# Performance work log

Measured on AMD Instinct MI355X. Metric: run time of the kernel, lower is better.

## Reference

```python
import jax, jax.numpy as jnp
import numpy as np

B, TE, TD = 16, 400, 64
E, H = 256, 512
H2 = 2 * H  # 1024
V = 32000


def setup_inputs():
    key = jax.random.key(0)
    k = jax.random.split(key, 16)
    s = 0.05
    return {
        "encoder_inputs": jax.random.randint(k[0], (B, TE), 0, V),
        "decoder_inputs": jax.random.randint(k[1], (B, TD), 0, V),
        "ext_oov_sizes": jax.random.randint(k[2], (B,), 0, 10),
        "enc_idxes_on_ext_voc": jax.random.randint(k[3], (B, TE), 0, V),
        "h0": jnp.zeros((2, B, H), jnp.float32),
        "c0": jnp.zeros((2, B, H), jnp.float32),
        "emb": jax.random.normal(k[4], (V, E)) * 0.1,
        "Wih_f": jax.random.normal(k[5], (4 * H, E)) * s,
        "Whh_f": jax.random.normal(k[6], (4 * H, H)) * s,
        "b_f": jnp.zeros((4 * H,), jnp.float32),
        "Wih_b": jax.random.normal(k[7], (4 * H, E)) * s,
        "Whh_b": jax.random.normal(k[8], (4 * H, H)) * s,
        "b_b": jnp.zeros((4 * H,), jnp.float32),
        "Wih_d": jax.random.normal(k[9], (4 * H2, E + 2 * H2)) * s,
        "Whh_d": jax.random.normal(k[10], (4 * H2, H2)) * s,
        "b_d": jnp.zeros((4 * H2,), jnp.float32),
        "W_ea": jax.random.normal(k[11], (H2, H2)) * 0.006,
        "W_da": jax.random.normal(k[12], (H2, H2)) * 0.006,
        "W_v": jax.random.normal(k[13], (V, 3 * H2)) * s,
        "b_v": jnp.zeros((V,), jnp.float32),
    }


def lstm_cell(x, h, c, Wih, Whh, b):
    z = x @ Wih.T + h @ Whh.T + b
    i, f, g, o = jnp.split(z, 4, axis=-1)
    i, f, o = jax.nn.sigmoid(i), jax.nn.sigmoid(f), jax.nn.sigmoid(o)
    c2 = f * c + i * jnp.tanh(g)
    return o * jnp.tanh(c2), c2


def run_lstm(xs, h0, c0, Wih, Whh, b):
    # xs: [T, B, E]
    def step(carry, x):
        h, c = lstm_cell(x, carry[0], carry[1], Wih, Whh, b)
        return (h, c), h
    (h, c), hs = jax.lax.scan(step, (h0, c0), xs)
    return hs, h, c


def _forward(emb, Wih_f, Whh_f, b_f, Wih_b, Whh_b, b_b, Wih_d, Whh_d, b_d,
             W_ea, W_da, W_v, b_v, h0, c0, encoder_inputs, decoder_inputs):
    xs = emb[encoder_inputs].transpose(1, 0, 2)  # [TE, B, E]
    hs_f, hf, cf = run_lstm(xs, h0[0], c0[0], Wih_f, Whh_f, b_f)
    hs_b, hb, cb = run_lstm(xs[::-1], h0[1], c0[1], Wih_b, Whh_b, b_b)
    enc_out = jnp.concatenate([hs_f, hs_b[::-1]], axis=-1).transpose(1, 0, 2)  # [B, TE, 2H]
    h = jnp.concatenate([hf, hb], axis=-1)  # [B, 2H] (torch reshape of bi-dir last hidden)
    c = jnp.concatenate([cf, cb], axis=-1)
    dec_emb = emb[decoder_inputs].transpose(1, 0, 2)  # [TD, B, E]

    def step(carry, xs_t):
        h, c, accum, buf = carry
        i, emb_t = xs_t
        # intra-temporal encoder attention: exp scores normalized by past accumulation
        scores = jnp.einsum('bd,btd->bt', h @ W_ea, enc_out)  # [B, TE]
        exp_s = jnp.exp(scores)
        denom = jnp.where(i == 0, jnp.ones_like(accum), accum)
        ep = exp_s / denom
        attn = ep / jnp.sum(ep, axis=-1, keepdims=True)
        ctx_e = jnp.einsum('bt,btd->bd', attn, enc_out)
        # intra-decoder attention over previously produced hidden states (masked)
        dsc = jnp.einsum('bd,tbd->bt', h @ W_da, buf)  # [B, TD]
        dsc = jnp.where((jnp.arange(TD) < i)[None, :], dsc, -1e30)
        dw = jnp.where(i == 0, 0.0, jax.nn.softmax(dsc, axis=-1))
        ctx_d = jnp.einsum('bt,tbd->bd', dw, buf)
        x = jnp.concatenate([emb_t, ctx_e, ctx_d], axis=-1)  # [B, E+4H]
        h2, c2 = lstm_cell(x, h, c, Wih_d, Whh_d, b_d)
        buf2 = buf.at[i].set(h2)
        feat = jnp.concatenate([h2, ctx_e, ctx_d], axis=-1)  # [B, 6H]
        logd = jax.nn.log_softmax(feat @ W_v.T + b_v, axis=-1)
        return (h2, c2, accum + exp_s, buf2), logd

    carry0 = (h, c, jnp.zeros((B, TE), h.dtype), jnp.zeros((TD, B, H2), h.dtype))
    (h, c, _, _), logds = jax.lax.scan(step, carry0, (jnp.arange(TD), dec_emb))
    return logds.transpose(1, 0, 2), h[None], c[None]


def reference(encoder_inputs, decoder_inputs, ext_oov_sizes, enc_idxes_on_ext_voc,
              h0, c0, emb, Wih_f, Whh_f, b_f, Wih_b, Whh_b, b_b,
              Wih_d, Whh_d, b_d, W_ea, W_da, W_v, b_v):
    # ext_oov_sizes / enc_idxes_on_ext_voc are unused by forward (as in the torch source)
    return _forward(emb, Wih_f, Whh_f, b_f, Wih_b, Whh_b, b_b, Wih_d, Whh_d, b_d,
                    W_ea, W_da, W_v, b_v, h0, c0, encoder_inputs, decoder_inputs)
```

## Files before the change

kernel.cpp:

```cpp
#include <hip/hip_runtime.h>
#include <math.h>

#define B_  16
#define TE_ 400
#define TD_ 64
#define E_  256
#define H_  512
#define H2_ 1024
#define V_  32000

typedef __attribute__((ext_vector_type(4))) float f32x4;
typedef __attribute__((ext_vector_type(8))) short s16x8;
typedef __attribute__((ext_vector_type(8))) unsigned short u16x8;
typedef __attribute__((ext_vector_type(4))) unsigned short u16x4;

__device__ __forceinline__ float bf2f(unsigned short u){
  union { unsigned int i; float f; } v; v.i = ((unsigned int)u) << 16; return v.f;
}
__device__ __forceinline__ unsigned short f2bf(float f){
  union { float f; unsigned int i; } v; v.f = f;
  return (unsigned short)((v.i + 0x7fffu + ((v.i >> 16) & 1u)) >> 16);
}
__device__ __forceinline__ float sigmoidf_(float x){ return 1.f/(1.f + expf(-x)); }

__device__ __forceinline__ void gl_lds16(const void* gsrc, void* ldst){
  __builtin_amdgcn_global_load_lds(
      (const __attribute__((address_space(1))) unsigned int*)gsrc,
      (__attribute__((address_space(3))) unsigned int*)ldst, 16, 0, 0);
}

__device__ __forceinline__ void arrive8(unsigned* inst){
  __threadfence();
  __hip_atomic_fetch_add(inst + (blockIdx.x & 7u)*16, 1u, __ATOMIC_RELAXED, __HIP_MEMORY_SCOPE_AGENT);
}
__device__ __forceinline__ void poll8(unsigned* inst, unsigned target){
  int it = 0;
  for(;;){
    unsigned s = 0;
    #pragma unroll
    for (int k = 0; k < 8; ++k)
      s += __hip_atomic_load(inst + k*16, __ATOMIC_RELAXED, __HIP_MEMORY_SCOPE_AGENT);
    if (s >= target) break;
    if (it < 6) __builtin_amdgcn_s_sleep(1);
    else if (it < 24) __builtin_amdgcn_s_sleep(4);
    else __builtin_amdgcn_s_sleep(16);
    ++it;
  }
}

__global__ void k_init(unsigned* bars, float* ctxn, float* psumT){
  int gid = blockIdx.x*256 + threadIdx.x;
  if (gid < 81920) bars[gid] = 0u;
  if (gid < 32768) ctxn[gid] = 0.f;
  if (gid < 32) psumT[gid] = 0.f;
}

__global__ void k_gather(const float* __restrict__ emb, const int* __restrict__ idx,
                         unsigned short* __restrict__ out, int T){
  int wv = threadIdx.x >> 6, l = threadIdx.x & 63;
  int row = blockIdx.x*4 + wv;
  if (row >= T*B_) return;
  int t = row >> 4, b = row & 15;
  int tok = idx[b*T + t];
  float4 v = *(const float4*)(emb + (size_t)tok*E_ + l*4);
  u16x4 o; o[0]=f2bf(v.x); o[1]=f2bf(v.y); o[2]=f2bf(v.z); o[3]=f2bf(v.w);
  *(u16x4*)(out + (size_t)row*E_ + l*4) = o;
}

__global__ void k_prep_enc(const float* __restrict__ Wih_f, const float* __restrict__ Whh_f,
                           const float* __restrict__ Wih_b, const float* __restrict__ Whh_b,
                           unsigned short* __restrict__ Wenc){
  int it = blockIdx.x*256 + threadIdx.x;
  int dir = it / (2048*96); int rem = it % (2048*96);
  int pr = rem / 96; int kc = rem % 96; int k0 = kc*8;
  int g = pr >> 6, r = pr & 63, gate = r >> 4, ul = r & 15;
  int orig = gate*H_ + g*16 + ul;
  const float* Wih = dir ? Wih_b : Wih_f;
  const float* Whh = dir ? Whh_b : Whh_f;
  u16x8 o;
  #pragma unroll
  for (int e = 0; e < 8; ++e){
    int k = k0 + e;
    float v = (k < E_) ? Wih[(size_t)orig*E_ + k] : Whh[(size_t)orig*H_ + (k - E_)];
    o[e] = f2bf(v);
  }
  *(u16x8*)(Wenc + ((size_t)dir*2048 + pr)*768 + k0) = o;
}

__device__ __forceinline__ void prep_whext_item(int it, const float* __restrict__ Whh_d,
                                                const float* __restrict__ W_da,
                                                char* __restrict__ WhExt){
  if (it < 524288){
    int g = it >> 13; int rem = it & 8191;
    int kblk = rem >> 10; int rem2 = rem & 1023;
    int row = rem2 >> 4; int k8 = rem2 & 15;
    int gate = row >> 4, ul = row & 15;
    int orig = gate*H2_ + g*16 + ul;
    u16x8 o;
    #pragma unroll
    for (int e = 0; e < 8; ++e)
      o[e] = f2bf(Whh_d[(size_t)orig*H2_ + kblk*128 + k8*8 + e]);
    size_t off = (size_t)g*163840 + (size_t)kblk*20480 + (size_t)(row*256 + ((k8*16) ^ ((row&7)<<4)));
    *(u16x8*)(WhExt + off) = o;
  } else if (it < 655360){
    int qi = it - 524288;
    int g = qi >> 11; int rem = qi & 2047;
    int kblk = rem >> 8; int c2 = rem & 255;
    int wvv = c2 >> 6, rr = (c2 >> 2) & 15, c = c2 & 3;
    int row = g*16 + rr;
    u16x8 o;
    #pragma unroll
    for (int e = 0; e < 8; ++e)
      o[e] = f2bf(W_da[(size_t)row*H2_ + kblk*128 + wvv*32 + c*8 + e]);
    size_t off = (size_t)g*163840 + (size_t)kblk*20480 + 16384
               + (size_t)(wvv*1024 + rr*64 + ((c*16) ^ ((rr&3)<<4)));
    *(u16x8*)(WhExt + off) = o;
  }
}

__device__ __forceinline__ void prep_ctx_item(int it, const float* __restrict__ Wih_d,
                                              char* __restrict__ CtxW){
  int g = it >> 14; int rem = it & 16383;
  int kblk = rem >> 10; int rem2 = rem & 1023;
  int row = rem2 >> 4; int k8 = rem2 & 15;
  int gate = row >> 4, ul = row & 15;
  int orig = gate*H2_ + g*16 + ul;
  int k = 256 + kblk*128 + k8*8;
  u16x8 o;
  #pragma unroll
  for (int e = 0; e < 8; ++e)
    o[e] = f2bf(Wih_d[(size_t)orig*2304 + k + e]);
  size_t off = (size_t)g*262144 + (size_t)kblk*16384 + (size_t)(row*256 + ((k8*16) ^ ((row&7)<<4)));
  *(u16x8*)(CtxW + off) = o;
}

__global__ void k_prep_wihemb(const float* __restrict__ Wih_d, unsigned short* __restrict__ Wemb){
  int it = blockIdx.x*256 + threadIdx.x;
  int p = it >> 5; int k0 = (it & 31)*8;
  int g = p >> 6, gate = (p >> 4) & 3, ul = p & 15;
  int orig = gate*H2_ + g*16 + ul;
  u16x8 o;
  #pragma unroll
  for (int e = 0; e < 8; ++e)
    o[e] = f2bf(Wih_d[(size_t)orig*2304 + k0 + e]);
  *(u16x8*)(Wemb + (size_t)p*256 + k0) = o;
}

__global__ void __launch_bounds__(256, 2) k_zinit(
    const unsigned short* __restrict__ A,
    const unsigned short* __restrict__ Bw,
    const float* __restrict__ bd,
    float* __restrict__ Cz)
{
  __shared__ unsigned short Ab[128*72];
  __shared__ unsigned short Bt[128*72];
  int p = blockIdx.x;
  int mt = p >> 5, nt = p & 31;
  int m0 = mt*128, n0 = nt*128;
  int tid = threadIdx.x, wvv = tid>>6, l = tid&63;
  int wr = wvv>>1, wc = wvv&1;
  f32x4 zero4 = {0.f,0.f,0.f,0.f};
  f32x4 acc[4][4];
  #pragma unroll
  for (int a=0;a<4;++a){
    #pragma unroll
    for (int b=0;b<4;++b) acc[a][b] = zero4;
  }
  for (int k0 = 0; k0 < 256; k0 += 64){
    #pragma unroll
    for (int qq = 0; qq < 4; ++qq){
      int idx8 = (tid + qq*256)*8;
      int r = idx8 >> 6, k = idx8 & 63;
      *(u16x8*)(Ab + r*72 + k) = *(const u16x8*)(A + (size_t)(m0+r)*256 + k0 + k);
      *(u16x8*)(Bt + r*72 + k) = *(const u16x8*)(Bw + (size_t)(n0+r)*256 + k0 + k);
    }
    __syncthreads();
    #pragma unroll
    for (int ks = 0; ks < 2; ++ks){
      s16x8 af[4], bf[4];
      #pragma unroll
      for (int fi=0;fi<4;++fi)
        af[fi] = *(const s16x8*)(Ab + (wr*64+fi*16+(l&15))*72 + ks*32 + (l>>4)*8);
      #pragma unroll
      for (int fj=0;fj<4;++fj)
        bf[fj] = *(const s16x8*)(Bt + (wc*64+fj*16+(l&15))*72 + ks*32 + (l>>4)*8);
      #pragma unroll
      for (int fi=0;fi<4;++fi){
        #pragma unroll
        for (int fj=0;fj<4;++fj)
          acc[fi][fj] = __builtin_amdgcn_mfma_f32_16x16x32_bf16(af[fi], bf[fj], acc[fi][fj], 0,0,0);
      }
    }
    __syncthreads();
  }
  #pragma unroll
  for (int fj=0;fj<4;++fj){
    int col = n0 + wc*64 + fj*16 + (l&15);
    int orig = ((col>>4)&3)*H2_ + (col>>6)*16 + (col&15);
    float bias = bd[orig];
    #pragma unroll
    for (int fi=0;fi<4;++fi){
      #pragma unroll
      for (int j=0;j<4;++j){
        int row = m0 + wr*64 + fi*16 + (l>>4)*4 + j;
        Cz[(size_t)row*4096 + col] = acc[fi][fj][j] + bias;
      }
    }
  }
}

__global__ void __launch_bounds__(256, 2) k_zx(
    const unsigned short* __restrict__ xs,
    const unsigned short* __restrict__ Wenc,
    const float* __restrict__ b_f, const float* __restrict__ b_b,
    unsigned short* __restrict__ zx)
{
  __shared__ unsigned short Ab[128*72];
  __shared__ unsigned short Bt[128*72];
  int pblk = blockIdx.x;
  int dir = pblk / 800; int rem = pblk % 800;
  int mt = rem >> 4, nt = rem & 15;
  int m0 = mt*128, n0 = nt*128;
  int tid = threadIdx.x, wvv = tid>>6, l = tid&63;
  int wr = wvv>>1, wc = wvv&1;
  f32x4 zero4 = {0.f,0.f,0.f,0.f};
  f32x4 acc[4][4];
  #pragma unroll
  for (int a=0;a<4;++a){
    #pragma unroll
    for (int b=0;b<4;++b) acc[a][b] = zero4;
  }
  for (int k0 = 0; k0 < 256; k0 += 64){
    #pragma unroll
    for (int qq = 0; qq < 4; ++qq){
      int idx8 = (tid + qq*256)*8;
      int r = idx8 >> 6, k = idx8 & 63;
      *(u16x8*)(Ab + r*72 + k) = *(const u16x8*)(xs + (size_t)(m0+r)*256 + k0 + k);
      *(u16x8*)(Bt + r*72 + k) = *(const u16x8*)(Wenc + ((size_t)dir*2048 + n0+r)*768 + k0 + k);
    }
    __syncthreads();
    #pragma unroll
    for (int ks = 0; ks < 2; ++ks){
      s16x8 af[4], bf[4];
      #pragma unroll
      for (int fi=0;fi<4;++fi)
        af[fi] = *(const s16x8*)(Ab + (wr*64+fi*16+(l&15))*72 + ks*32 + (l>>4)*8);
      #pragma unroll
      for (int fj=0;fj<4;++fj)
        bf[fj] = *(const s16x8*)(Bt + (wc*64+fj*16+(l&15))*72 + ks*32 + (l>>4)*8);
      #pragma unroll
      for (int fi=0;fi<4;++fi){
        #pragma unroll
        for (int fj=0;fj<4;++fj)
          acc[fi][fj] = __builtin_amdgcn_mfma_f32_16x16x32_bf16(af[fi], bf[fj], acc[fi][fj], 0,0,0);
      }
    }
    __syncthreads();
  }
  const float* bsrc = dir ? b_b : b_f;
  #pragma unroll
  for (int fj=0;fj<4;++fj){
    int col = n0 + wc*64 + fj*16 + (l&15);
    float bias = bsrc[((col>>4)&3)*512 + (col>>6)*16 + (col&15)];
    #pragma unroll
    for (int fi=0;fi<4;++fi){
      #pragma unroll
      for (int j=0;j<4;++j){
        int row = m0 + wr*64 + fi*16 + (l>>4)*4 + j;
        zx[((size_t)dir*6400 + row)*2048 + col] = f2bf(acc[fi][fj][j] + bias);
      }
    }
  }
}

__global__ void __launch_bounds__(256, 2) k_penc(
    const unsigned short* __restrict__ enc,
    const float* __restrict__ Wea,
    unsigned short* __restrict__ P)
{
  __shared__ unsigned short Ab[128*72];
  __shared__ unsigned short Bt[128*72];
  int p = blockIdx.x;
  int mt = p >> 3, nt = p & 7;
  int m0 = mt*128, n0 = nt*128;
  int tid = threadIdx.x, wvv = tid>>6, l = tid&63;
  int wr = wvv>>1, wc = wvv&1;
  f32x4 zero4 = {0.f,0.f,0.f,0.f};
  f32x4 acc[4][4];
  #pragma unroll
  for (int a=0;a<4;++a){
    #pragma unroll
    for (int b=0;b<4;++b) acc[a][b] = zero4;
  }
  for (int k0 = 0; k0 < 1024; k0 += 64){
    #pragma unroll
    for (int qq = 0; qq < 4; ++qq){
      int idx8 = (tid + qq*256)*8;
      int r = idx8 >> 6, k = idx8 & 63;
      *(u16x8*)(Ab + r*72 + k) = *(const u16x8*)(enc + (size_t)(m0+r)*1024 + k0 + k);
    }
    #pragma unroll
    for (int qq = 0; qq < 4; ++qq){
      int idx8 = (tid + qq*256)*8;
      int r = idx8 >> 6, k = idx8 & 63;
      const float* src = Wea + (size_t)(n0+r)*1024 + k0 + k;
      float4 v0 = *(const float4*)src;
      float4 v1 = *(const float4*)(src+4);
      u16x8 o;
      o[0]=f2bf(v0.x); o[1]=f2bf(v0.y); o[2]=f2bf(v0.z); o[3]=f2bf(v0.w);
      o[4]=f2bf(v1.x); o[5]=f2bf(v1.y); o[6]=f2bf(v1.z); o[7]=f2bf(v1.w);
      *(u16x8*)(Bt + r*72 + k) = o;
    }
    __syncthreads();
    #pragma unroll
    for (int ks = 0; ks < 2; ++ks){
      s16x8 af[4], bf[4];
      #pragma unroll
      for (int fi=0;fi<4;++fi)
        af[fi] = *(const s16x8*)(Ab + (wr*64+fi*16+(l&15))*72 + ks*32 + (l>>4)*8);
      #pragma unroll
      for (int fj=0;fj<4;++fj)
        bf[fj] = *(const s16x8*)(Bt + (wc*64+fj*16+(l&15))*72 + ks*32 + (l>>4)*8);
      #pragma unroll
      for (int fi=0;fi<4;++fi){
        #pragma unroll
        for (int fj=0;fj<4;++fj)
          acc[fi][fj] = __builtin_amdgcn_mfma_f32_16x16x32_bf16(af[fi], bf[fj], acc[fi][fj], 0,0,0);
      }
    }
    __syncthreads();
  }
  #pragma unroll
  for (int fj=0;fj<4;++fj){
    int col = n0 + wc*64 + fj*16 + (l&15);
    #pragma unroll
    for (int fi=0;fi<4;++fi){
      #pragma unroll
      for (int j=0;j<4;++j){
        int row = m0 + wr*64 + fi*16 + (l>>4)*4 + j;
        P[(size_t)row*1024 + col] = f2bf(acc[fi][fj][j]);
      }
    }
  }
}

__global__ void __launch_bounds__(256, 1) k_encoder(
    const unsigned short* __restrict__ zx,
    const unsigned short* __restrict__ Wenc,
    const float* __restrict__ h0, const float* __restrict__ c0,
    unsigned short* __restrict__ enc_out,
    unsigned short* __restrict__ hbuf,
    float* __restrict__ h0dec, float* __restrict__ c0dec,
    unsigned* __restrict__ bars,
    const float* __restrict__ Whh_d, const float* __restrict__ W_da,
    const float* __restrict__ Wih_d,
    char* __restrict__ WhExt, char* __restrict__ CtxW)
{
  extern __shared__ char smem[];
  int tid = threadIdx.x;
  int w = blockIdx.x;
  if (w >= 64){
    int base = (w - 64)*256 + tid;
    for (int it = base; it < 655360; it += 36864) prep_whext_item(it, Whh_d, W_da, WhExt);
    for (int it = base; it < 1048576; it += 36864) prep_ctx_item(it, Wih_d, CtxW);
    return;
  }
  unsigned short* Wt = (unsigned short*)smem;
  unsigned short* At = Wt + 64*520;
  float* zl = (float*)(At + 16*520);
  int dir = w >> 5, g = w & 31;
  int wv = tid >> 6, l = tid & 63;
  {
    const unsigned short* Wsrc = Wenc + ((size_t)dir*2048 + g*64)*768 + 256;
    int r = tid >> 2, s = tid & 3;
    for (int c = 0; c < 16; ++c)
      *(u16x8*)(Wt + r*520 + s*128 + c*8) = *(const u16x8*)(Wsrc + (size_t)r*768 + s*128 + c*8);
  }
  int bb = tid >> 4, ul = tid & 15;
  float creg = c0[((size_t)dir*16 + bb)*H_ + g*16 + ul];
  int kchunk = (l >> 4) * 8;
  f32x4 zero4 = { 0.f, 0.f, 0.f, 0.f };
  {
    int r = tid >> 4, s = tid & 15;
    for (int e = 0; e < 32; ++e)
      At[r*520 + s*32 + e] = f2bf(h0[((size_t)dir*16 + r)*H_ + s*32 + e]);
  }
  int tg0 = dir ? (TE_-1) : 0;
  const unsigned short* zrow = zx + ((size_t)dir*6400 + (size_t)tg0*16 + (l>>4)*4)*2048 + g*64 + wv*16 + (l&15);
  f32x4 a0cur;
  a0cur[0]=bf2f(zrow[0]); a0cur[1]=bf2f(zrow[2048]); a0cur[2]=bf2f(zrow[4096]); a0cur[3]=bf2f(zrow[6144]);
  __syncthreads();
  for (int t = 0; t < TE_; ++t){
    int tg = dir ? (TE_-1 - t) : t;
    f32x4 acc0 = a0cur, acc1 = zero4;
    const unsigned short* brow = Wt + (wv*16 + (l&15))*520 + kchunk;
    const unsigned short* ap   = At + (l&15)*520 + kchunk;
    #pragma unroll
    for (int ks = 0; ks < 16; ++ks){
      s16x8 afr = *(const s16x8*)(ap + ks*32);
      s16x8 bfr = *(const s16x8*)(brow + ks*32);
      if (ks & 1) acc1 = __builtin_amdgcn_mfma_f32_16x16x32_bf16(afr, bfr, acc1, 0, 0, 0);
      else        acc0 = __builtin_amdgcn_mfma_f32_16x16x32_bf16(afr, bfr, acc0, 0, 0, 0);
    }
    f32x4 acc = acc0 + acc1;
    #pragma unroll
    for (int j = 0; j < 4; ++j)
      zl[wv*256 + ((l>>4)*4 + j)*16 + (l&15)] = acc[j];
    __syncthreads();
    float zi = zl[0*256 + bb*16 + ul];
    float zf = zl[1*256 + bb*16 + ul];
    float zg = zl[2*256 + bb*16 + ul];
    float zo = zl[3*256 + bb*16 + ul];
    float iv = sigmoidf_(zi), fv = sigmoidf_(zf), gv = tanhf(zg), ov = sigmoidf_(zo);
    float cc = fv*creg + iv*gv;
    float hh = ov * tanhf(cc);
    creg = cc;
    int u = g*16 + ul;
    unsigned short hb = f2bf(hh);
    hbuf[((size_t)dir*2 + ((t+1)&1))*(16*H_) + bb*H_ + u] = hb;
    enc_out[((size_t)bb*TE_ + tg)*H2_ + dir*H_ + u] = hb;
    if (t == TE_-1){
      h0dec[(size_t)bb*H2_ + dir*H_ + u] = hh;
      c0dec[(size_t)bb*H2_ + dir*H_ + u] = cc;
    }
    unsigned* cnt = bars + (size_t)(dir*400 + t)*64;
    __syncthreads();
    if (tid == 0){
      __threadfence();
      __hip_atomic_fetch_add(cnt + (g&3)*16, 1u, __ATOMIC_RELAXED, __HIP_MEMORY_SCOPE_AGENT);
    }
    if (t+1 < TE_){
      int tg2 = dir ? (TE_-2 - t) : (t+1);
      const unsigned short* zr2 = zx + ((size_t)dir*6400 + (size_t)tg2*16 + (l>>4)*4)*2048 + g*64 + wv*16 + (l&15);
      a0cur[0]=bf2f(zr2[0]); a0cur[1]=bf2f(zr2[2048]); a0cur[2]=bf2f(zr2[4096]); a0cur[3]=bf2f(zr2[6144]);
    }
    if (tid == 0){
      int it = 0;
      for(;;){
        unsigned s_ = 0;
        #pragma unroll
        for (int k2 = 0; k2 < 4; ++k2)
          s_ += __hip_atomic_load(cnt + k2*16, __ATOMIC_RELAXED, __HIP_MEMORY_SCOPE_AGENT);
        if (s_ >= 32) break;
        if (it < 6) __builtin_amdgcn_s_sleep(1);
        else __builtin_amdgcn_s_sleep(4);
        ++it;
      }
      __threadfence();
    }
    __syncthreads();
    if (t+1 < TE_){
      int r = tid >> 4, s = tid & 15;
      const unsigned short* hsrc = hbuf + ((size_t)dir*2 + ((t+1)&1))*(16*H_) + r*H_ + s*32;
      for (int c = 0; c < 4; ++c)
        *(u16x8*)(At + r*520 + s*32 + c*8) = *(const u16x8*)(hsrc + c*8);
    }
    __syncthreads();
  }
}

__global__ void k_dec_init(const float* __restrict__ h0dec, unsigned short* __restrict__ hreg){
  int gid = blockIdx.x*256 + threadIdx.x;
  if (gid < 16384) hreg[gid] = f2bf(h0dec[gid]);
}

__device__ __forceinline__ void issueA(const char* gA, char* BbA, int wv, int l, int kblk, int buf){
  const char* gsrc = gA + (size_t)kblk*20480;
  char* lb = BbA + buf*20480;
  #pragma unroll
  for (int q = 0; q < 4; ++q)
    gl_lds16(gsrc + wv*4096 + q*1024 + (size_t)l*16, lb + wv*4096 + q*1024);
  gl_lds16(gsrc + 16384 + wv*1024 + (size_t)l*16, lb + 16384 + wv*1024);
}
__device__ __forceinline__ void issueC(const char* gC, char* BbC, int wv, int l, int kblk, int buf){
  const char* gsrc = gC + (size_t)kblk*16384;
  char* lb = BbC + buf*16384;
  #pragma unroll
  for (int q = 0; q < 4; ++q)
    gl_lds16(gsrc + wv*4096 + q*1024 + (size_t)l*16, lb + wv*4096 + q*1024);
}

__global__ void __launch_bounds__(256, 1) k_decoder(
  const char* __restrict__ WhExt,
  const char* __restrict__ CtxW,
  const float* __restrict__ zinit,
  const unsigned short* __restrict__ Penc,
  const unsigned short* __restrict__ enc_out,
  const float* __restrict__ c0dec,
  unsigned short* __restrict__ hreg,
  unsigned short* __restrict__ xbuf,
  float* __restrict__ ctxn,
  float* __restrict__ psumT,
  unsigned short* __restrict__ vbuf,
  unsigned short* __restrict__ bufh,
  unsigned short* __restrict__ Av,
  float* __restrict__ outHC,
  unsigned* __restrict__ bars)
{
  extern __shared__ char smem[];
  int tid = threadIdx.x, w = blockIdx.x;
  int wv = tid >> 6, l = tid & 63;
  unsigned* dbase = bars + 51200;

  unsigned short* Atc = (unsigned short*)smem;
  unsigned short* Ah  = (unsigned short*)smem;
  char* BbA = smem + 66560;
  char* BbC = smem + 128000;
  float* zq = (float*)(smem + 66560);
  float* zl = (float*)(smem + 128000);
  unsigned short* encL = (unsigned short*)smem;
  float* epL  = (float*)(smem + 103424);
  float* accL = (float*)(smem + 103680);
  float* dscL = (float*)smem;

  bool isZ = (w < 64);
  bool isE = (w >= 64 && w < 192);
  int eb = 0, ec = 0;
  if (isE){ eb = (w-64) >> 3; ec = (w-64) & 7; }
  int db = w - 192;

  if (isE){
    for (int rr = 0; rr < 50; ++rr){
      const unsigned short* src = enc_out + ((size_t)eb*TE_ + ec*50 + rr)*H2_;
      *(u16x4*)(encL + rr*1032 + tid*4) = *(const u16x4*)(src + tid*4);
    }
    if (tid < 50) accL[tid] = 0.f;
    __syncthreads();
  }
  float creg = 0.f;
  int bb = tid >> 4, ul = tid & 15;
  const char* gA = WhExt + (size_t)w*163840;
  const char* gC = CtxW + (size_t)w*262144;
  f32x4 acc0, acc1;

  for (int i = 0; i < TD_; ++i){
    int p = i & 1;
    unsigned* barM = dbase + (size_t)(i*3+0)*128;
    unsigned* barA = dbase + (size_t)(i*3+1)*128;
    unsigned* barB = dbase + (size_t)(i*3+2)*128;

    if (isZ){
      ctxn[(p^1)*16384 + w*256 + tid] = 0.f;
      if (w == 0 && tid < 16) psumT[(p^1)*16 + tid] = 0.f;
      const float* zsrc = zinit + ((size_t)i*16 + (l>>4)*4)*4096 + w*64 + wv*16 + (l&15);
      f32x4 a0i; a0i[0]=zsrc[0]; a0i[1]=zsrc[4096]; a0i[2]=zsrc[8192]; a0i[3]=zsrc[12288];
      issueA(gA, BbA, wv, l, 0, 0);
      issueA(gA, BbA, wv, l, 1, 1);
      {
        int r = tid >> 4, s = tid & 15;
        const unsigned short* hsrc = hreg + p*16384 + r*H2_ + s*64;
        for (int c = 0; c < 8; ++c)
          *(u16x8*)(Ah + r*1032 + s*64 + c*8) = *(const u16x8*)(hsrc + c*8);
      }
      __syncthreads();
      acc0 = a0i;
      f32x4 z4 = {0.f,0.f,0.f,0.f};
      acc1 = z4;
      f32x4 accv = z4;
      int swz = ((l&7)<<4);
      for (int kblk = 0; kblk < 8; ++kblk){
        int buf = kblk % 3;
        if (kblk + 2 < 8) issueA(gA, BbA, wv, l, kblk+2, (kblk+2)%3);
        if (kblk < 6)       asm volatile("s_waitcnt vmcnt(10)" ::: "memory");
        else if (kblk == 6) asm volatile("s_waitcnt vmcnt(5)" ::: "memory");
        else                asm volatile("s_waitcnt vmcnt(0)" ::: "memory");
        const unsigned short* ap = Ah + (l&15)*1032 + kblk*128 + (l>>4)*8;
        const char* Bz = BbA + buf*20480 + wv*4096;
        #pragma unroll
        for (int ks = 0; ks < 4; ++ks){
          int k8 = ks*4 + (l>>4);
          s16x8 afr = *(const s16x8*)(ap + ks*32);
          s16x8 bfr = *(const s16x8*)(Bz + (l&15)*256 + ((k8*16) ^ swz));
          if (ks & 1) acc1 = __builtin_amdgcn_mfma_f32_16x16x32_bf16(afr, bfr, acc1, 0,0,0);
          else        acc0 = __builtin_amdgcn_mfma_f32_16x16x32_bf16(afr, bfr, acc0, 0,0,0);
        }
        s16x8 afq = *(const s16x8*)(Ah + (l&15)*1032 + kblk*128 + wv*32 + (l>>4)*8);
        s16x8 bfv = *(const s16x8*)(BbA + buf*20480 + 16384 + wv*1024 + (l&15)*64 + ((((l>>4)*16)) ^ ((l&3)<<4)));
        accv = __builtin_amdgcn_mfma_f32_16x16x32_bf16(afq, bfv, accv, 0,0,0);
      }
      __syncthreads();
      #pragma unroll
      for (int j = 0; j < 4; ++j)
        zq[wv*256 + ((l>>4)*4+j)*16 + (l&15)] = accv[j];
      __syncthreads();
      if (i > 0){
        float vv = zq[0*256+bb*16+ul] + zq[1*256+bb*16+ul] + zq[2*256+bb*16+ul] + zq[3*256+bb*16+ul];
        vbuf[((size_t)(i-1)*16 + bb)*H2_ + w*16 + ul] = f2bf(vv);
      }
      __syncthreads();
      if (tid == 0) arrive8(barM);
      issueC(gC, BbC, wv, l, 0, 0);
      issueC(gC, BbC, wv, l, 1, 1);
      if (tid == 0){ poll8(barA, 144); __threadfence(); }
      __syncthreads();
      {
        int r = tid >> 4, s = tid & 15;
        float inv = 1.f / psumT[p*16 + r];
        const float* cn = ctxn + p*16384 + (size_t)r*1024 + s*64;
        for (int c8 = 0; c8 < 8; ++c8){
          float4 v0 = *(const float4*)(cn + c8*8);
          float4 v1 = *(const float4*)(cn + c8*8 + 4);
          u16x8 o;
          o[0]=f2bf(v0.x*inv); o[1]=f2bf(v0.y*inv); o[2]=f2bf(v0.z*inv); o[3]=f2bf(v0.w*inv);
          o[4]=f2bf(v1.x*inv); o[5]=f2bf(v1.y*inv); o[6]=f2bf(v1.z*inv); o[7]=f2bf(v1.w*inv);
          *(u16x8*)(Atc + r*2056 + s*64 + c8*8) = o;
        }
        const unsigned short* xd = xbuf + (size_t)r*1024 + s*64;
        for (int c8 = 0; c8 < 8; ++c8)
          *(u16x8*)(Atc + r*2056 + 1024 + s*64 + c8*8) = *(const u16x8*)(xd + c8*8);
      }
      {
        float val = ctxn[p*16384 + (size_t)bb*1024 + w*16 + ul] / psumT[p*16 + bb];
        Av[((size_t)bb*TD_ + i)*3072 + 1024 + w*16 + ul] = f2bf(val);
      }
      __syncthreads();
      for (int k = 0; k < 16; ++k){
        if (k < 15) asm volatile("s_waitcnt vmcnt(4)" ::: "memory");
        else        asm volatile("s_waitcnt vmcnt(0)" ::: "memory");
        const unsigned short* ap = Atc + (l&15)*2056 + k*128 + (l>>4)*8;
        const char* Bz = BbC + (k&1)*16384 + wv*4096;
        #pragma unroll
        for (int ks = 0; ks < 4; ++ks){
          int k8 = ks*4 + (l>>4);
          s16x8 afr = *(const s16x8*)(ap + ks*32);
          s16x8 bfr = *(const s16x8*)(Bz + (l&15)*256 + ((k8*16) ^ swz));
          if (ks & 1) acc1 = __builtin_amdgcn_mfma_f32_16x16x32_bf16(afr, bfr, acc1, 0,0,0);
          else        acc0 = __builtin_amdgcn_mfma_f32_16x16x32_bf16(afr, bfr, acc0, 0,0,0);
        }
        if (k + 2 < 16) issueC(gC, BbC, wv, l, k+2, k&1);
      }
      __syncthreads();
      f32x4 acc = acc0 + acc1;
      #pragma unroll
      for (int j = 0; j < 4; ++j)
        zl[wv*256 + ((l>>4)*4+j)*16 + (l&15)] = acc[j];
      __syncthreads();
      float zi = zl[0*256 + bb*16 + ul];
      float zf = zl[1*256 + bb*16 + ul];
      float zg = zl[2*256 + bb*16 + ul];
      float zo = zl[3*256 + bb*16 + ul];
      if (i == 0) creg = c0dec[(size_t)bb*H2_ + w*16 + ul];
      float iv = sigmoidf_(zi), fv = sigmoidf_(zf), gv = tanhf(zg), ov = sigmoidf_(zo);
      float cc = fv*creg + iv*gv;
      float hh = ov*tanhf(cc);
      creg = cc;
      int u = w*16 + ul;
      unsigned short hb2 = f2bf(hh);
      hreg[((i+1)&1)*16384 + (size_t)bb*H2_ + u] = hb2;
      Av[((size_t)bb*TD_ + i)*3072 + u] = hb2;
      bufh[((size_t)i*16 + bb)*H2_ + u] = hb2;
      if (i == TD_-1){
        outHC[(size_t)bb*H2_ + u] = hh;
        outHC[16384 + (size_t)bb*H2_ + u] = cc;
      }
      __syncthreads();
      if (tid == 0){ arrive8(barB); poll8(barB, 64); __threadfence(); }
      __syncthreads();
    } else if (isE){
      const unsigned short* hb_ = hreg + p*16384 + eb*H2_ + l*16;
      u16x8 hv0 = *(const u16x8*)hb_;
      u16x8 hv1 = *(const u16x8*)(hb_ + 8);
      float hf[16];
      #pragma unroll
      for (int c = 0; c < 8; ++c){ hf[c] = bf2f(hv0[c]); hf[8+c] = bf2f(hv1[c]); }
      for (int rr = wv; rr < 50; rr += 4){
        const unsigned short* pr = Penc + ((size_t)(eb*TE_ + ec*50 + rr))*H2_ + l*16;
        u16x8 p0 = *(const u16x8*)pr;
        u16x8 p1 = *(const u16x8*)(pr + 8);
        float sc = 0.f;
        #pragma unroll
        for (int c = 0; c < 8; ++c) sc += hf[c]*bf2f(p0[c]);
        #pragma unroll
        for (int c = 0; c < 8; ++c) sc += hf[8+c]*bf2f(p1[c]);
        #pragma unroll
        for (int o = 1; o < 64; o <<= 1) sc += __shfl_xor(sc, o);
        if (l == 0){
          float es = expf(sc);
          float aold = accL[rr];
          float denom = (i == 0) ? 1.f : aold;
          accL[rr] = aold + es;
          epL[rr] = es / denom;
        }
      }
      __syncthreads();
      float tot = 0.f;
      for (int rr = 0; rr < 50; ++rr) tot += epL[rr];
      float a0=0.f,a1=0.f,a2=0.f,a3=0.f;
      for (int rr = 0; rr < 50; ++rr){
        float wgt = epL[rr];
        u16x4 ev = *(const u16x4*)(encL + rr*1032 + tid*4);
        a0 += wgt*bf2f(ev[0]); a1 += wgt*bf2f(ev[1]); a2 += wgt*bf2f(ev[2]); a3 += wgt*bf2f(ev[3]);
      }
      float* dst = ctxn + p*16384 + (size_t)eb*1024 + tid*4;
      atomicAdd(dst+0, a0); atomicAdd(dst+1, a1); atomicAdd(dst+2, a2); atomicAdd(dst+3, a3);
      if (tid == 0) atomicAdd(psumT + p*16 + eb, tot);
      __syncthreads();
      if (tid == 0){ arrive8(barA); poll8(barB, 64); __threadfence(); }
      __syncthreads();
    } else {
      int col = tid*4;
      if (i == 0){
        u16x4 z4v = {0,0,0,0};
        *(u16x4*)(xbuf + (size_t)db*1024 + col) = z4v;
        *(u16x4*)(Av + ((size_t)db*TD_ + i)*3072 + 2048 + col) = z4v;
      } else {
        if (tid == 0){ poll8(barM, 64); __threadfence(); }
        __syncthreads();
        const unsigned short* hq = hreg + p*16384 + db*H2_ + l*16;
        u16x8 h0v = *(const u16x8*)hq;
        u16x8 h1v = *(const u16x8*)(hq + 8);
        float qf[16];
        #pragma unroll
        for (int c = 0; c < 8; ++c){ qf[c] = bf2f(h0v[c]); qf[8+c] = bf2f(h1v[c]); }
        for (int tp = wv; tp < i; tp += 4){
          const unsigned short* vr = vbuf + ((size_t)tp*16 + db)*H2_ + l*16;
          u16x8 e0 = *(const u16x8*)vr;
          u16x8 e1 = *(const u16x8*)(vr + 8);
          float sc = 0.f;
          #pragma unroll
          for (int c = 0; c < 8; ++c) sc += qf[c]*bf2f(e0[c]);
          #pragma unroll
          for (int c = 0; c < 8; ++c) sc += qf[8+c]*bf2f(e1[c]);
          #pragma unroll
          for (int o = 1; o < 64; o <<= 1) sc += __shfl_xor(sc, o);
          if (l == 0) dscL[tp] = sc;
        }
        __syncthreads();
        float scv = (l < i) ? dscL[l] : -1e30f;
        float m = scv;
        #pragma unroll
        for (int o = 1; o < 64; o <<= 1) m = fmaxf(m, __shfl_xor(m, o));
        float e = (l < i) ? expf(scv - m) : 0.f;
        float ssum = e;
        #pragma unroll
        for (int o = 1; o < 64; o <<= 1) ssum += __shfl_xor(ssum, o);
        float wgt = e / ssum;
        float c0_=0.f,c1_=0.f,c2_=0.f,c3_=0.f;
        for (int tp = 0; tp < i; ++tp){
          float wt = __shfl(wgt, tp);
          u16x4 hv = *(const u16x4*)(bufh + ((size_t)tp*16 + db)*H2_ + col);
          c0_ += wt*bf2f(hv[0]); c1_ += wt*bf2f(hv[1]); c2_ += wt*bf2f(hv[2]); c3_ += wt*bf2f(hv[3]);
        }
        u16x4 o4; o4[0]=f2bf(c0_); o4[1]=f2bf(c1_); o4[2]=f2bf(c2_); o4[3]=f2bf(c3_);
        *(u16x4*)(xbuf + (size_t)db*1024 + col) = o4;
        *(u16x4*)(Av + ((size_t)db*TD_ + i)*3072 + 2048 + col) = o4;
      }
      __syncthreads();
      if (tid == 0){ arrive8(barA); poll8(barB, 64); __threadfence(); }
      __syncthreads();
    }
  }
}

__global__ void __launch_bounds__(256, 2) k_vocab_gemm(
    const unsigned short* __restrict__ Av,
    const float* __restrict__ Wv,
    const float* __restrict__ bv,
    float* __restrict__ out)
{
  __shared__ unsigned short Ab[128*72];
  __shared__ unsigned short Bt[128*72];
  int p = blockIdx.x;
  int mt = (p>>3)&7, nt = (p&7) + 8*(p>>6);
  if (nt >= 250) return;
  int m0 = mt*128, n0 = nt*128;
  int tid = threadIdx.x, wvv = tid>>6, l = tid&63;
  int wr = wvv>>1, wc = wvv&1;
  f32x4 zero4 = {0.f,0.f,0.f,0.f};
  f32x4 acc[4][4];
  #pragma unroll
  for (int a=0;a<4;++a){
    #pragma unroll
    for (int b=0;b<4;++b) acc[a][b] = zero4;
  }
  for (int k0 = 0; k0 < 3072; k0 += 64){
    #pragma unroll
    for (int qq = 0; qq < 4; ++qq){
      int idx8 = (tid + qq*256)*8;
      int r = idx8 >> 6, k = idx8 & 63;
      *(u16x8*)(Ab + r*72 + k) = *(const u16x8*)(Av + (size_t)(m0+r)*3072 + k0 + k);
    }
    #pragma unroll
    for (int qq = 0; qq < 4; ++qq){
      int idx8 = (tid + qq*256)*8;
      int r = idx8 >> 6, k = idx8 & 63;
      const float* src = Wv + (size_t)(n0+r)*3072 + k0 + k;
      float4 v0 = *(const float4*)src;
      float4 v1 = *(const float4*)(src+4);
      u16x8 o;
      o[0]=f2bf(v0.x); o[1]=f2bf(v0.y); o[2]=f2bf(v0.z); o[3]=f2bf(v0.w);
      o[4]=f2bf(v1.x); o[5]=f2bf(v1.y); o[6]=f2bf(v1.z); o[7]=f2bf(v1.w);
      *(u16x8*)(Bt + r*72 + k) = o;
    }
    __syncthreads();
    #pragma unroll
    for (int ks = 0; ks < 2; ++ks){
      s16x8 af[4], bf[4];
      #pragma unroll
      for (int fi=0;fi<4;++fi)
        af[fi] = *(const s16x8*)(Ab + (wr*64+fi*16+(l&15))*72 + ks*32 + (l>>4)*8);
      #pragma unroll
      for (int fj=0;fj<4;++fj)
        bf[fj] = *(const s16x8*)(Bt + (wc*64+fj*16+(l&15))*72 + ks*32 + (l>>4)*8);
      #pragma unroll
      for (int fi=0;fi<4;++fi){
        #pragma unroll
        for (int fj=0;fj<4;++fj)
          acc[fi][fj] = __builtin_amdgcn_mfma_f32_16x16x32_bf16(af[fi], bf[fj], acc[fi][fj], 0,0,0);
      }
    }
    __syncthreads();
  }
  #pragma unroll
  for (int fj=0;fj<4;++fj){
    int col = n0 + wc*64 + fj*16 + (l&15);
    float bias = bv[col];
    #pragma unroll
    for (int fi=0;fi<4;++fi){
      #pragma unroll
      for (int j=0;j<4;++j){
        int row = m0 + wr*64 + fi*16 + (l>>4)*4 + j;
        out[(size_t)row*V_ + col] = acc[fi][fj][j] + bias;
      }
    }
  }
}

__global__ void k_logsoftmax(float* __restrict__ out){
  int row = blockIdx.x;
  float* x = out + (size_t)row*V_;
  int tid = threadIdx.x;
  __shared__ float red[64];
  float m = -1e30f;
  for (int c = tid; c < V_; c += 256) m = fmaxf(m, x[c]);
  #pragma unroll
  for (int o=1;o<64;o<<=1) m = fmaxf(m, __shfl_xor(m,o));
  if ((tid&63)==0) red[tid>>6] = m;
  __syncthreads();
  m = fmaxf(fmaxf(red[0],red[1]), fmaxf(red[2],red[3]));
  float s = 0.f;
  for (int c = tid; c < V_; c += 256) s += expf(x[c]-m);
  #pragma unroll
  for (int o=1;o<64;o<<=1) s += __shfl_xor(s,o);
  if ((tid&63)==0) red[8 + (tid>>6)] = s;
  __syncthreads();
  s = red[8]+red[9]+red[10]+red[11];
  float lse = m + logf(s);
  for (int c = tid; c < V_; c += 256) x[c] = x[c] - lse;
}

extern "C" void kernel_launch(void* const* d_in, const int* in_sizes, int n_in,
                              void* d_out, int out_size, void* d_ws, size_t ws_size,
                              hipStream_t stream){
  (void)in_sizes; (void)n_in; (void)out_size; (void)ws_size;
  const int*   enc_in = (const int*)d_in[0];
  const int*   dec_in = (const int*)d_in[1];
  const float* h0   = (const float*)d_in[4];
  const float* c0   = (const float*)d_in[5];
  const float* emb  = (const float*)d_in[6];
  const float* Wih_f= (const float*)d_in[7];
  const float* Whh_f= (const float*)d_in[8];
  const float* b_f  = (const float*)d_in[9];
  const float* Wih_b= (const float*)d_in[10];
  const float* Whh_b= (const float*)d_in[11];
  const float* b_b  = (const float*)d_in[12];
  const float* Wih_d= (const float*)d_in[13];
  const float* Whh_d= (const float*)d_in[14];
  const float* b_d  = (const float*)d_in[15];
  const float* W_ea = (const float*)d_in[16];
  const float* W_da = (const float*)d_in[17];
  const float* W_v  = (const float*)d_in[18];
  const float* b_v  = (const float*)d_in[19];
  float* out = (float*)d_out;
  char* ws = (char*)d_ws;

  size_t o_bars   = 0;
  size_t o_ctxn   = 327680;
  size_t o_psumT  = o_ctxn + 131072;
  size_t o_xs     = o_psumT + 256;
  size_t o_decemb = o_xs + (size_t)6400*256*2;
  size_t o_Wenc   = o_decemb + (size_t)1024*256*2;
  size_t o_WhExt  = o_Wenc + (size_t)2*2048*768*2;
  size_t o_CtxW   = o_WhExt + (size_t)64*163840;
  size_t o_Wemb   = o_CtxW + (size_t)64*262144;
  size_t o_zinit  = o_Wemb + (size_t)4096*256*2;
  size_t o_zx     = o_zinit + (size_t)1024*4096*4;
  size_t o_enc    = o_zx + (size_t)2*6400*2048*2;
  size_t o_Penc   = o_enc + (size_t)16*400*1024*2;
  size_t o_hbuf   = o_Penc + (size_t)16*400*1024*2;
  size_t o_h0dec  = o_hbuf + (size_t)2*2*16*512*2;
  size_t o_c0dec  = o_h0dec + (size_t)16*1024*4;
  size_t o_hreg   = o_c0dec + (size_t)16*1024*4;
  size_t o_xbuf   = o_hreg + (size_t)2*16*1024*2;
  size_t o_vbuf   = o_xbuf + (size_t)16*1024*2;
  size_t o_bufh   = o_vbuf + (size_t)64*16*1024*2;
  size_t o_Av     = o_bufh + (size_t)64*16*1024*2;

  unsigned* bars        = (unsigned*)(ws + o_bars);
  float* ctxn           = (float*)(ws + o_ctxn);
  float* psumT          = (float*)(ws + o_psumT);
  unsigned short* xs    = (unsigned short*)(ws + o_xs);
  unsigned short* decemb= (unsigned short*)(ws + o_decemb);
  unsigned short* Wenc  = (unsigned short*)(ws + o_Wenc);
  char* WhExt           = ws + o_WhExt;
  char* CtxW            = ws + o_CtxW;
  unsigned short* Wemb  = (unsigned short*)(ws + o_Wemb);
  float* zinit          = (float*)(ws + o_zinit);
  unsigned short* zx    = (unsigned short*)(ws + o_zx);
  unsigned short* encO  = (unsigned short*)(ws + o_enc);
  unsigned short* Penc  = (unsigned short*)(ws + o_Penc);
  unsigned short* hbuf  = (unsigned short*)(ws + o_hbuf);
  float* h0dec          = (float*)(ws + o_h0dec);
  float* c0dec          = (float*)(ws + o_c0dec);
  unsigned short* hreg  = (unsigned short*)(ws + o_hreg);
  unsigned short* xbuf  = (unsigned short*)(ws + o_xbuf);
  unsigned short* vbuf  = (unsigned short*)(ws + o_vbuf);
  unsigned short* bufh  = (unsigned short*)(ws + o_bufh);
  unsigned short* Av    = (unsigned short*)(ws + o_Av);

  hipFuncSetAttribute((const void*)k_encoder, hipFuncAttributeMaxDynamicSharedMemorySize, 90000);
  hipFuncSetAttribute((const void*)k_decoder, hipFuncAttributeMaxDynamicSharedMemorySize, 160768);

  k_init<<<320, 256, 0, stream>>>(bars, ctxn, psumT);
  k_gather<<<1600, 256, 0, stream>>>(emb, enc_in, xs, TE_);
  k_gather<<<256, 256, 0, stream>>>(emb, dec_in, decemb, TD_);
  k_prep_enc<<<1536, 256, 0, stream>>>(Wih_f, Whh_f, Wih_b, Whh_b, Wenc);
  k_prep_wihemb<<<512, 256, 0, stream>>>(Wih_d, Wemb);
  k_zinit<<<256, 256, 0, stream>>>(decemb, Wemb, b_d, zinit);
  k_zx<<<1600, 256, 0, stream>>>(xs, Wenc, b_f, b_b, zx);
  k_encoder<<<208, 256, 87296, stream>>>(zx, Wenc, h0, c0, encO, hbuf, h0dec, c0dec, bars,
                                         Whh_d, W_da, Wih_d, WhExt, CtxW);
  k_penc<<<400, 256, 0, stream>>>(encO, W_ea, Penc);
  k_dec_init<<<64, 256, 0, stream>>>(h0dec, hreg);
  k_decoder<<<208, 256, 160768, stream>>>(WhExt, CtxW, zinit, Penc, encO, c0dec,
                                          hreg, xbuf, ctxn, psumT, vbuf, bufh, Av,
                                          out + (size_t)32768000, bars);
  k_vocab_gemm<<<2048, 256, 0, stream>>>(Av, W_v, b_v, out);
  k_logsoftmax<<<1024, 256, 0, stream>>>(out);
}
```

Measured before the change: 5.538 ms.

## Restructure decoder into 256 uniform blocks with resident Whh slices

The decoder moves from a 208-block heterogeneous split (gate-GEMM, attention and decoder-attention roles) to 256 uniform blocks. Each block owns 4 hidden units, keeps its Whh_d slice and its slice of the projected encoder output in LDS, and streams its context weights each step. The W_da projection becomes an fp32 dot product with cross-lane reductions instead of an MFMA tile. Barrier counters are re-laid out per instance and spread over 8 slots, and weight prep and permutations are rewritten to match. This targets per-step latency and load imbalance in the serial decoder loop, at the cost of more blocks joining each grid barrier and scalar fp32 work in place of MFMA.

```diff
diff --git a/kernel.cpp b/kernel.cpp
--- a/kernel.cpp
+++ b/kernel.cpp
@@ -28,29 +28,35 @@
       (const __attribute__((address_space(1))) unsigned int*)gsrc,
       (__attribute__((address_space(3))) unsigned int*)ldst, 16, 0, 0);
 }
-
-__device__ __forceinline__ void arrive8(unsigned* inst){
+__device__ __forceinline__ void issue4(const char* gsrc, char* ldst, int l){
+  #pragma unroll
+  for (int q = 0; q < 4; ++q)
+    gl_lds16(gsrc + q*1024 + (size_t)l*16, ldst + q*1024);
+}
+
+__device__ __forceinline__ void d_arrive(unsigned* bars, int inst){
   __threadfence();
-  __hip_atomic_fetch_add(inst + (blockIdx.x & 7u)*16, 1u, __ATOMIC_RELAXED, __HIP_MEMORY_SCOPE_AGENT);
-}
-__device__ __forceinline__ void poll8(unsigned* inst, unsigned target){
+  __hip_atomic_fetch_add(bars + (blockIdx.x & 7u)*4096 + inst*16, 1u, __ATOMIC_RELAXED, __HIP_MEMORY_SCOPE_AGENT);
+}
+__device__ __forceinline__ void d_poll(unsigned* bars, int inst, unsigned tgt){
   int it = 0;
   for(;;){
     unsigned s = 0;
     #pragma unroll
     for (int k = 0; k < 8; ++k)
-      s += __hip_atomic_load(inst + k*16, __ATOMIC_RELAXED, __HIP_MEMORY_SCOPE_AGENT);
-    if (s >= target) break;
+      s += __hip_atomic_load(bars + k*4096 + inst*16, __ATOMIC_RELAXED, __HIP_MEMORY_SCOPE_AGENT);
+    if (s >= tgt) break;
     if (it < 6) __builtin_amdgcn_s_sleep(1);
     else if (it < 24) __builtin_amdgcn_s_sleep(4);
     else __builtin_amdgcn_s_sleep(16);
     ++it;
   }
+  __threadfence();
 }
 
 __global__ void k_init(unsigned* bars, float* ctxn, float* psumT){
   int gid = blockIdx.x*256 + threadIdx.x;
-  if (gid < 81920) bars[gid] = 0u;
+  if (gid < 99328) bars[gid] = 0u;
   if (gid < 32768) ctxn[gid] = 0.f;
   if (gid < 32) psumT[gid] = 0.f;
 }
@@ -87,58 +93,38 @@
   *(u16x8*)(Wenc + ((size_t)dir*2048 + pr)*768 + k0) = o;
 }
 
-__device__ __forceinline__ void prep_whext_item(int it, const float* __restrict__ Whh_d,
-                                                const float* __restrict__ W_da,
-                                                char* __restrict__ WhExt){
-  if (it < 524288){
-    int g = it >> 13; int rem = it & 8191;
-    int kblk = rem >> 10; int rem2 = rem & 1023;
-    int row = rem2 >> 4; int k8 = rem2 & 15;
-    int gate = row >> 4, ul = row & 15;
-    int orig = gate*H2_ + g*16 + ul;
-    u16x8 o;
-    #pragma unroll
-    for (int e = 0; e < 8; ++e)
-      o[e] = f2bf(Whh_d[(size_t)orig*H2_ + kblk*128 + k8*8 + e]);
-    size_t off = (size_t)g*163840 + (size_t)kblk*20480 + (size_t)(row*256 + ((k8*16) ^ ((row&7)<<4)));
-    *(u16x8*)(WhExt + off) = o;
-  } else if (it < 655360){
-    int qi = it - 524288;
-    int g = qi >> 11; int rem = qi & 2047;
-    int kblk = rem >> 8; int c2 = rem & 255;
-    int wvv = c2 >> 6, rr = (c2 >> 2) & 15, c = c2 & 3;
-    int row = g*16 + rr;
-    u16x8 o;
-    #pragma unroll
-    for (int e = 0; e < 8; ++e)
-      o[e] = f2bf(W_da[(size_t)row*H2_ + kblk*128 + wvv*32 + c*8 + e]);
-    size_t off = (size_t)g*163840 + (size_t)kblk*20480 + 16384
-               + (size_t)(wvv*1024 + rr*64 + ((c*16) ^ ((rr&3)<<4)));
-    *(u16x8*)(WhExt + off) = o;
-  }
-}
-
-__device__ __forceinline__ void prep_ctx_item(int it, const float* __restrict__ Wih_d,
-                                              char* __restrict__ CtxW){
-  int g = it >> 14; int rem = it & 16383;
-  int kblk = rem >> 10; int rem2 = rem & 1023;
-  int row = rem2 >> 4; int k8 = rem2 & 15;
-  int gate = row >> 4, ul = row & 15;
-  int orig = gate*H2_ + g*16 + ul;
-  int k = 256 + kblk*128 + k8*8;
+__device__ __forceinline__ void prep_rwhh_item(int it, const float* __restrict__ Whh_d,
+                                               char* __restrict__ RW){
+  int w = it >> 11; int rem = it & 2047;
+  int sb = rem >> 8; int e = rem & 255;
+  int row = e >> 4, k8 = e & 15;
+  int orig = (row >> 2)*H2_ + w*4 + (row & 3);
   u16x8 o;
   #pragma unroll
-  for (int e = 0; e < 8; ++e)
-    o[e] = f2bf(Wih_d[(size_t)orig*2304 + k + e]);
-  size_t off = (size_t)g*262144 + (size_t)kblk*16384 + (size_t)(row*256 + ((k8*16) ^ ((row&7)<<4)));
-  *(u16x8*)(CtxW + off) = o;
+  for (int e2 = 0; e2 < 8; ++e2)
+    o[e2] = f2bf(Whh_d[(size_t)orig*H2_ + sb*128 + k8*8 + e2]);
+  size_t off = (size_t)w*32768 + (size_t)sb*4096 + (size_t)(row*256 + ((k8*16) ^ ((row&7)<<4)));
+  *(u16x8*)(RW + off) = o;
+}
+__device__ __forceinline__ void prep_rwctx_item(int it, const float* __restrict__ Wih_d,
+                                                char* __restrict__ RC){
+  int w = it >> 12; int rem = it & 4095;
+  int sb = rem >> 8; int e = rem & 255;
+  int row = e >> 4, k8 = e & 15;
+  int orig = (row >> 2)*H2_ + w*4 + (row & 3);
+  int col = 256 + sb*128 + k8*8;
+  u16x8 o;
+  #pragma unroll
+  for (int e2 = 0; e2 < 8; ++e2)
+    o[e2] = f2bf(Wih_d[(size_t)orig*2304 + col + e2]);
+  size_t off = (size_t)w*65536 + (size_t)sb*4096 + (size_t)(row*256 + ((k8*16) ^ ((row&7)<<4)));
+  *(u16x8*)(RC + off) = o;
 }
 
 __global__ void k_prep_wihemb(const float* __restrict__ Wih_d, unsigned short* __restrict__ Wemb){
   int it = blockIdx.x*256 + threadIdx.x;
   int p = it >> 5; int k0 = (it & 31)*8;
-  int g = p >> 6, gate = (p >> 4) & 3, ul = p & 15;
-  int orig = gate*H2_ + g*16 + ul;
+  int orig = ((p>>2)&3)*H2_ + (p>>4)*4 + (p&3);
   u16x8 o;
   #pragma unroll
   for (int e = 0; e < 8; ++e)
@@ -196,7 +182,7 @@
   #pragma unroll
   for (int fj=0;fj<4;++fj){
     int col = n0 + wc*64 + fj*16 + (l&15);
-    int orig = ((col>>4)&3)*H2_ + (col>>6)*16 + (col&15);
+    int orig = ((col>>2)&3)*H2_ + (col>>4)*4 + (col&3);
     float bias = bd[orig];
     #pragma unroll
     for (int fi=0;fi<4;++fi){
@@ -352,17 +338,16 @@
     unsigned short* __restrict__ hbuf,
     float* __restrict__ h0dec, float* __restrict__ c0dec,
     unsigned* __restrict__ bars,
-    const float* __restrict__ Whh_d, const float* __restrict__ W_da,
-    const float* __restrict__ Wih_d,
-    char* __restrict__ WhExt, char* __restrict__ CtxW)
+    const float* __restrict__ Whh_d, const float* __restrict__ Wih_d,
+    char* __restrict__ RWhhG, char* __restrict__ RWctxG)
 {
   extern __shared__ char smem[];
   int tid = threadIdx.x;
   int w = blockIdx.x;
   if (w >= 64){
     int base = (w - 64)*256 + tid;
-    for (int it = base; it < 655360; it += 36864) prep_whext_item(it, Whh_d, W_da, WhExt);
-    for (int it = base; it < 1048576; it += 36864) prep_ctx_item(it, Wih_d, CtxW);
+    for (int it = base; it < 524288; it += 36864) prep_rwhh_item(it, Whh_d, RWhhG);
+    for (int it = base; it < 1048576; it += 36864) prep_rwctx_item(it, Wih_d, RWctxG);
     return;
   }
   unsigned short* Wt = (unsigned short*)smem;
@@ -370,6 +355,7 @@
   float* zl = (float*)(At + 16*520);
   int dir = w >> 5, g = w & 31;
   int wv = tid >> 6, l = tid & 63;
+  unsigned* ebars = bars + 32768;
   {
     const unsigned short* Wsrc = Wenc + ((size_t)dir*2048 + g*64)*768 + 256;
     int r = tid >> 2, s = tid & 3;
@@ -423,11 +409,11 @@
       h0dec[(size_t)bb*H2_ + dir*H_ + u] = hh;
       c0dec[(size_t)bb*H2_ + dir*H_ + u] = cc;
     }
-    unsigned* cnt = bars + (size_t)(dir*400 + t)*64;
+    int inst = dir*400 + t;
     __syncthreads();
     if (tid == 0){
       __threadfence();
-      __hip_atomic_fetch_add(cnt + (g&3)*16, 1u, __ATOMIC_RELAXED, __HIP_MEMORY_SCOPE_AGENT);
+      __hip_atomic_fetch_add(ebars + (g&3)*16384 + inst*16, 1u, __ATOMIC_RELAXED, __HIP_MEMORY_SCOPE_AGENT);
     }
     if (t+1 < TE_){
       int tg2 = dir ? (TE_-2 - t) : (t+1);
@@ -440,7 +426,7 @@
         unsigned s_ = 0;
         #pragma unroll
         for (int k2 = 0; k2 < 4; ++k2)
-          s_ += __hip_atomic_load(cnt + k2*16, __ATOMIC_RELAXED, __HIP_MEMORY_SCOPE_AGENT);
+          s_ += __hip_atomic_load(ebars + k2*16384 + inst*16, __ATOMIC_RELAXED, __HIP_MEMORY_SCOPE_AGENT);
         if (s_ >= 32) break;
         if (it < 6) __builtin_amdgcn_s_sleep(1);
         else __builtin_amdgcn_s_sleep(4);
@@ -464,28 +450,21 @@
   if (gid < 16384) hreg[gid] = f2bf(h0dec[gid]);
 }
 
-__device__ __forceinline__ void issueA(const char* gA, char* BbA, int wv, int l, int kblk, int buf){
-  const char* gsrc = gA + (size_t)kblk*20480;
-  char* lb = BbA + buf*20480;
-  #pragma unroll
-  for (int q = 0; q < 4; ++q)
-    gl_lds16(gsrc + wv*4096 + q*1024 + (size_t)l*16, lb + wv*4096 + q*1024);
-  gl_lds16(gsrc + 16384 + wv*1024 + (size_t)l*16, lb + 16384 + wv*1024);
-}
-__device__ __forceinline__ void issueC(const char* gC, char* BbC, int wv, int l, int kblk, int buf){
-  const char* gsrc = gC + (size_t)kblk*16384;
-  char* lb = BbC + buf*16384;
-  #pragma unroll
-  for (int q = 0; q < 4; ++q)
-    gl_lds16(gsrc + wv*4096 + q*1024 + (size_t)l*16, lb + wv*4096 + q*1024);
-}
+#define OFF_PENC  32768
+#define OFF_WB    83968
+#define OFF_ZL    149504
+#define OFF_EPL   157696
+#define OFF_ACCL  157824
+#define OFF_DSCL  157952
+#define DEC_SMEM  158208
 
 __global__ void __launch_bounds__(256, 1) k_decoder(
-  const char* __restrict__ WhExt,
-  const char* __restrict__ CtxW,
+  const char* __restrict__ RWhhG,
+  const char* __restrict__ RWctxG,
   const float* __restrict__ zinit,
   const unsigned short* __restrict__ Penc,
   const unsigned short* __restrict__ enc_out,
+  const float* __restrict__ W_da,
   const float* __restrict__ c0dec,
   unsigned short* __restrict__ hreg,
   unsigned short* __restrict__ xbuf,
@@ -498,180 +477,120 @@
   unsigned* __restrict__ bars)
 {
   extern __shared__ char smem[];
+  char* RW = smem;
+  unsigned short* PencL = (unsigned short*)(smem + OFF_PENC);
+  char* WB = smem + OFF_WB;
+  float* zl   = (float*)(smem + OFF_ZL);
+  float* epL  = (float*)(smem + OFF_EPL);
+  float* accL = (float*)(smem + OFF_ACCL);
+  float* dscL = (float*)(smem + OFF_DSCL);
+
   int tid = threadIdx.x, w = blockIdx.x;
   int wv = tid >> 6, l = tid & 63;
-  unsigned* dbase = bars + 51200;
-
-  unsigned short* Atc = (unsigned short*)smem;
-  unsigned short* Ah  = (unsigned short*)smem;
-  char* BbA = smem + 66560;
-  char* BbC = smem + 128000;
-  float* zq = (float*)(smem + 66560);
-  float* zl = (float*)(smem + 128000);
-  unsigned short* encL = (unsigned short*)smem;
-  float* epL  = (float*)(smem + 103424);
-  float* accL = (float*)(smem + 103680);
-  float* dscL = (float*)smem;
-
-  bool isZ = (w < 64);
-  bool isE = (w >= 64 && w < 192);
-  int eb = 0, ec = 0;
-  if (isE){ eb = (w-64) >> 3; ec = (w-64) & 7; }
-  int db = w - 192;
-
-  if (isE){
-    for (int rr = 0; rr < 50; ++rr){
-      const unsigned short* src = enc_out + ((size_t)eb*TE_ + ec*50 + rr)*H2_;
-      *(u16x4*)(encL + rr*1032 + tid*4) = *(const u16x4*)(src + tid*4);
-    }
-    if (tid < 50) accL[tid] = 0.f;
-    __syncthreads();
-  }
+  int b_att = w >> 4, tr = w & 15;
+  bool isDec = ((w & 3) == 0);
+  int qd = (w >> 2) & 3, b_dec = w >> 4;
+  int swz = ((l&7)<<4);
+
+  {
+    const float4* src = (const float4*)(RWhhG + (size_t)w*32768);
+    float4* dst = (float4*)RW;
+    for (int o = tid; o < 2048; o += 256) dst[o] = src[o];
+    const float4* ps = (const float4*)(Penc + ((size_t)b_att*400 + tr*25)*1024);
+    float4* pd = (float4*)PencL;
+    for (int o = tid; o < 3200; o += 256) pd[o] = ps[o];
+  }
+  if (tid < 25) accL[tid] = 0.f;
   float creg = 0.f;
-  int bb = tid >> 4, ul = tid & 15;
-  const char* gA = WhExt + (size_t)w*163840;
-  const char* gC = CtxW + (size_t)w*262144;
-  f32x4 acc0, acc1;
+  if (tid < 64) creg = c0dec[(size_t)(tid>>2)*H2_ + w*4 + (tid&3)];
+  __syncthreads();
+
+  const char* gWB = RWctxG + (size_t)w*65536;
+  char* myWB = WB + wv*16384;
 
   for (int i = 0; i < TD_; ++i){
     int p = i & 1;
-    unsigned* barM = dbase + (size_t)(i*3+0)*128;
-    unsigned* barA = dbase + (size_t)(i*3+1)*128;
-    unsigned* barB = dbase + (size_t)(i*3+2)*128;
-
-    if (isZ){
+    int instV = i*3, instX = i*3+1, instY = i*3+2;
+    if (w < 64){
       ctxn[(p^1)*16384 + w*256 + tid] = 0.f;
       if (w == 0 && tid < 16) psumT[(p^1)*16 + tid] = 0.f;
-      const float* zsrc = zinit + ((size_t)i*16 + (l>>4)*4)*4096 + w*64 + wv*16 + (l&15);
-      f32x4 a0i; a0i[0]=zsrc[0]; a0i[1]=zsrc[4096]; a0i[2]=zsrc[8192]; a0i[3]=zsrc[12288];
-      issueA(gA, BbA, wv, l, 0, 0);
-      issueA(gA, BbA, wv, l, 1, 1);
-      {
-        int r = tid >> 4, s = tid & 15;
-        const unsigned short* hsrc = hreg + p*16384 + r*H2_ + s*64;
-        for (int c = 0; c < 8; ++c)
-          *(u16x8*)(Ah + r*1032 + s*64 + c*8) = *(const u16x8*)(hsrc + c*8);
-      }
-      __syncthreads();
-      acc0 = a0i;
+    }
+    issue4(gWB + (size_t)(2*wv+0)*4096, myWB + 0*4096, l);
+    issue4(gWB + (size_t)(2*wv+1)*4096, myWB + 1*4096, l);
+    issue4(gWB + (size_t)(8+2*wv)*4096, myWB + 2*4096, l);
+    issue4(gWB + (size_t)(9+2*wv)*4096, myWB + 3*4096, l);
+    if (i > 0){
+      for (int bi = 0; bi < 4; ++bi){
+        int b2 = wv*4 + bi;
+        const unsigned short* hp = hreg + p*16384 + (size_t)b2*H2_ + l*16;
+        u16x8 hv0 = *(const u16x8*)hp;
+        u16x8 hv1 = *(const u16x8*)(hp + 8);
+        float hfl[16];
+        #pragma unroll
+        for (int e = 0; e < 8; ++e){ hfl[e] = bf2f(hv0[e]); hfl[8+e] = bf2f(hv1[e]); }
+        #pragma unroll
+        for (int jl = 0; jl < 4; ++jl){
+          const float* wr = W_da + (size_t)(w*4+jl)*H2_ + l*16;
+          float4 w0 = *(const float4*)(wr);
+          float4 w1 = *(const float4*)(wr+4);
+          float4 w2 = *(const float4*)(wr+8);
+          float4 w3 = *(const float4*)(wr+12);
+          float s = hfl[0]*w0.x + hfl[1]*w0.y + hfl[2]*w0.z + hfl[3]*w0.w
+                  + hfl[4]*w1.x + hfl[5]*w1.y + hfl[6]*w1.z + hfl[7]*w1.w
+                  + hfl[8]*w2.x + hfl[9]*w2.y + hfl[10]*w2.z + hfl[11]*w2.w
+                  + hfl[12]*w3.x + hfl[13]*w3.y + hfl[14]*w3.z + hfl[15]*w3.w;
+          #pragma unroll
+          for (int o = 1; o < 64; o <<= 1) s += __shfl_xor(s, o);
+          if (l == 0) vbuf[((size_t)(i-1)*16 + b2)*H2_ + w*4 + jl] = f2bf(s);
+        }
+      }
+    }
+    if (tid == 0) d_arrive(bars, instV);
+    f32x4 accz0, accz1;
+    {
       f32x4 z4 = {0.f,0.f,0.f,0.f};
-      acc1 = z4;
-      f32x4 accv = z4;
-      int swz = ((l&7)<<4);
-      for (int kblk = 0; kblk < 8; ++kblk){
-        int buf = kblk % 3;
-        if (kblk + 2 < 8) issueA(gA, BbA, wv, l, kblk+2, (kblk+2)%3);
-        if (kblk < 6)       asm volatile("s_waitcnt vmcnt(10)" ::: "memory");
-        else if (kblk == 6) asm volatile("s_waitcnt vmcnt(5)" ::: "memory");
-        else                asm volatile("s_waitcnt vmcnt(0)" ::: "memory");
-        const unsigned short* ap = Ah + (l&15)*1032 + kblk*128 + (l>>4)*8;
-        const char* Bz = BbA + buf*20480 + wv*4096;
-        #pragma unroll
-        for (int ks = 0; ks < 4; ++ks){
-          int k8 = ks*4 + (l>>4);
-          s16x8 afr = *(const s16x8*)(ap + ks*32);
-          s16x8 bfr = *(const s16x8*)(Bz + (l&15)*256 + ((k8*16) ^ swz));
-          if (ks & 1) acc1 = __builtin_amdgcn_mfma_f32_16x16x32_bf16(afr, bfr, acc1, 0,0,0);
-          else        acc0 = __builtin_amdgcn_mfma_f32_16x16x32_bf16(afr, bfr, acc0, 0,0,0);
-        }
-        s16x8 afq = *(const s16x8*)(Ah + (l&15)*1032 + kblk*128 + wv*32 + (l>>4)*8);
-        s16x8 bfv = *(const s16x8*)(BbA + buf*20480 + 16384 + wv*1024 + (l&15)*64 + ((((l>>4)*16)) ^ ((l&3)<<4)));
-        accv = __builtin_amdgcn_mfma_f32_16x16x32_bf16(afq, bfv, accv, 0,0,0);
-      }
-      __syncthreads();
-      #pragma unroll
-      for (int j = 0; j < 4; ++j)
-        zq[wv*256 + ((l>>4)*4+j)*16 + (l&15)] = accv[j];
-      __syncthreads();
-      if (i > 0){
-        float vv = zq[0*256+bb*16+ul] + zq[1*256+bb*16+ul] + zq[2*256+bb*16+ul] + zq[3*256+bb*16+ul];
-        vbuf[((size_t)(i-1)*16 + bb)*H2_ + w*16 + ul] = f2bf(vv);
-      }
-      __syncthreads();
-      if (tid == 0) arrive8(barM);
-      issueC(gC, BbC, wv, l, 0, 0);
-      issueC(gC, BbC, wv, l, 1, 1);
-      if (tid == 0){ poll8(barA, 144); __threadfence(); }
-      __syncthreads();
-      {
-        int r = tid >> 4, s = tid & 15;
-        float inv = 1.f / psumT[p*16 + r];
-        const float* cn = ctxn + p*16384 + (size_t)r*1024 + s*64;
-        for (int c8 = 0; c8 < 8; ++c8){
-          float4 v0 = *(const float4*)(cn + c8*8);
-          float4 v1 = *(const float4*)(cn + c8*8 + 4);
-          u16x8 o;
-          o[0]=f2bf(v0.x*inv); o[1]=f2bf(v0.y*inv); o[2]=f2bf(v0.z*inv); o[3]=f2bf(v0.w*inv);
-          o[4]=f2bf(v1.x*inv); o[5]=f2bf(v1.y*inv); o[6]=f2bf(v1.z*inv); o[7]=f2bf(v1.w*inv);
-          *(u16x8*)(Atc + r*2056 + s*64 + c8*8) = o;
-        }
-        const unsigned short* xd = xbuf + (size_t)r*1024 + s*64;
-        for (int c8 = 0; c8 < 8; ++c8)
-          *(u16x8*)(Atc + r*2056 + 1024 + s*64 + c8*8) = *(const u16x8*)(xd + c8*8);
-      }
-      {
-        float val = ctxn[p*16384 + (size_t)bb*1024 + w*16 + ul] / psumT[p*16 + bb];
-        Av[((size_t)bb*TD_ + i)*3072 + 1024 + w*16 + ul] = f2bf(val);
-      }
-      __syncthreads();
-      for (int k = 0; k < 16; ++k){
-        if (k < 15) asm volatile("s_waitcnt vmcnt(4)" ::: "memory");
-        else        asm volatile("s_waitcnt vmcnt(0)" ::: "memory");
-        const unsigned short* ap = Atc + (l&15)*2056 + k*128 + (l>>4)*8;
-        const char* Bz = BbC + (k&1)*16384 + wv*4096;
-        #pragma unroll
-        for (int ks = 0; ks < 4; ++ks){
-          int k8 = ks*4 + (l>>4);
-          s16x8 afr = *(const s16x8*)(ap + ks*32);
-          s16x8 bfr = *(const s16x8*)(Bz + (l&15)*256 + ((k8*16) ^ swz));
-          if (ks & 1) acc1 = __builtin_amdgcn_mfma_f32_16x16x32_bf16(afr, bfr, acc1, 0,0,0);
-          else        acc0 = __builtin_amdgcn_mfma_f32_16x16x32_bf16(afr, bfr, acc0, 0,0,0);
-        }
-        if (k + 2 < 16) issueC(gC, BbC, wv, l, k+2, k&1);
-      }
-      __syncthreads();
-      f32x4 acc = acc0 + acc1;
-      #pragma unroll
-      for (int j = 0; j < 4; ++j)
-        zl[wv*256 + ((l>>4)*4+j)*16 + (l&15)] = acc[j];
-      __syncthreads();
-      float zi = zl[0*256 + bb*16 + ul];
-      float zf = zl[1*256 + bb*16 + ul];
-      float zg = zl[2*256 + bb*16 + ul];
-      float zo = zl[3*256 + bb*16 + ul];
-      if (i == 0) creg = c0dec[(size_t)bb*H2_ + w*16 + ul];
-      float iv = sigmoidf_(zi), fv = sigmoidf_(zf), gv = tanhf(zg), ov = sigmoidf_(zo);
-      float cc = fv*creg + iv*gv;
-      float hh = ov*tanhf(cc);
-      creg = cc;
-      int u = w*16 + ul;
-      unsigned short hb2 = f2bf(hh);
-      hreg[((i+1)&1)*16384 + (size_t)bb*H2_ + u] = hb2;
-      Av[((size_t)bb*TD_ + i)*3072 + u] = hb2;
-      bufh[((size_t)i*16 + bb)*H2_ + u] = hb2;
-      if (i == TD_-1){
-        outHC[(size_t)bb*H2_ + u] = hh;
-        outHC[16384 + (size_t)bb*H2_ + u] = cc;
-      }
-      __syncthreads();
-      if (tid == 0){ arrive8(barB); poll8(barB, 64); __threadfence(); }
-      __syncthreads();
-    } else if (isE){
-      const unsigned short* hb_ = hreg + p*16384 + eb*H2_ + l*16;
-      u16x8 hv0 = *(const u16x8*)hb_;
-      u16x8 hv1 = *(const u16x8*)(hb_ + 8);
+      accz1 = z4;
+      if (wv == 0){
+        const float* zsrc = zinit + ((size_t)i*16)*4096 + w*16 + (l&15);
+        f32x4 a;
+        a[0] = zsrc[(size_t)((l>>4)*4+0)*4096];
+        a[1] = zsrc[(size_t)((l>>4)*4+1)*4096];
+        a[2] = zsrc[(size_t)((l>>4)*4+2)*4096];
+        a[3] = zsrc[(size_t)((l>>4)*4+3)*4096];
+        accz0 = a;
+      } else accz0 = z4;
+    }
+    {
+      int kbase = wv*256;
+      s16x8 af[8];
+      #pragma unroll
+      for (int ks = 0; ks < 8; ++ks)
+        af[ks] = *(const s16x8*)(hreg + p*16384 + (size_t)(l&15)*H2_ + kbase + ks*32 + (l>>4)*8);
+      #pragma unroll
+      for (int ks = 0; ks < 8; ++ks){
+        const char* sbL = RW + (size_t)(2*wv + (ks>>2))*4096;
+        int k8 = (ks&3)*4 + (l>>4);
+        s16x8 bfr = *(const s16x8*)(sbL + (l&15)*256 + ((k8*16) ^ swz));
+        if (ks & 1) accz1 = __builtin_amdgcn_mfma_f32_16x16x32_bf16(af[ks], bfr, accz1, 0,0,0);
+        else        accz0 = __builtin_amdgcn_mfma_f32_16x16x32_bf16(af[ks], bfr, accz0, 0,0,0);
+      }
+    }
+    {
+      const unsigned short* hp = hreg + p*16384 + (size_t)b_att*H2_ + l*16;
+      u16x8 hv0 = *(const u16x8*)hp;
+      u16x8 hv1 = *(const u16x8*)(hp + 8);
       float hf[16];
       #pragma unroll
-      for (int c = 0; c < 8; ++c){ hf[c] = bf2f(hv0[c]); hf[8+c] = bf2f(hv1[c]); }
-      for (int rr = wv; rr < 50; rr += 4){
-        const unsigned short* pr = Penc + ((size_t)(eb*TE_ + ec*50 + rr))*H2_ + l*16;
+      for (int e = 0; e < 8; ++e){ hf[e] = bf2f(hv0[e]); hf[8+e] = bf2f(hv1[e]); }
+      for (int rr = wv; rr < 25; rr += 4){
+        const unsigned short* pr = PencL + rr*1024 + l*16;
         u16x8 p0 = *(const u16x8*)pr;
         u16x8 p1 = *(const u16x8*)(pr + 8);
         float sc = 0.f;
         #pragma unroll
-        for (int c = 0; c < 8; ++c) sc += hf[c]*bf2f(p0[c]);
-        #pragma unroll
-        for (int c = 0; c < 8; ++c) sc += hf[8+c]*bf2f(p1[c]);
+        for (int e = 0; e < 8; ++e) sc += hf[e]*bf2f(p0[e]);
+        #pragma unroll
+        for (int e = 0; e < 8; ++e) sc += hf[8+e]*bf2f(p1[e]);
         #pragma unroll
         for (int o = 1; o < 64; o <<= 1) sc += __shfl_xor(sc, o);
         if (l == 0){
@@ -684,71 +603,135 @@
       }
       __syncthreads();
       float tot = 0.f;
-      for (int rr = 0; rr < 50; ++rr) tot += epL[rr];
+      for (int rr = 0; rr < 25; ++rr) tot += epL[rr];
       float a0=0.f,a1=0.f,a2=0.f,a3=0.f;
-      for (int rr = 0; rr < 50; ++rr){
+      const unsigned short* ebase = enc_out + ((size_t)b_att*TE_ + tr*25)*H2_ + tid*4;
+      for (int rr = 0; rr < 25; ++rr){
         float wgt = epL[rr];
-        u16x4 ev = *(const u16x4*)(encL + rr*1032 + tid*4);
+        u16x4 ev = *(const u16x4*)(ebase + (size_t)rr*H2_);
         a0 += wgt*bf2f(ev[0]); a1 += wgt*bf2f(ev[1]); a2 += wgt*bf2f(ev[2]); a3 += wgt*bf2f(ev[3]);
       }
-      float* dst = ctxn + p*16384 + (size_t)eb*1024 + tid*4;
+      float* dst = ctxn + p*16384 + (size_t)b_att*H2_ + tid*4;
       atomicAdd(dst+0, a0); atomicAdd(dst+1, a1); atomicAdd(dst+2, a2); atomicAdd(dst+3, a3);
-      if (tid == 0) atomicAdd(psumT + p*16 + eb, tot);
-      __syncthreads();
-      if (tid == 0){ arrive8(barA); poll8(barB, 64); __threadfence(); }
-      __syncthreads();
-    } else {
-      int col = tid*4;
+      if (tid == 0) atomicAdd(psumT + p*16 + b_att, tot);
+    }
+    if (isDec){
+      int col = qd*256 + tid;
       if (i == 0){
-        u16x4 z4v = {0,0,0,0};
-        *(u16x4*)(xbuf + (size_t)db*1024 + col) = z4v;
-        *(u16x4*)(Av + ((size_t)db*TD_ + i)*3072 + 2048 + col) = z4v;
+        xbuf[(size_t)b_dec*H2_ + col] = 0;
+        Av[((size_t)b_dec*TD_ + i)*3072 + 2048 + col] = 0;
       } else {
-        if (tid == 0){ poll8(barM, 64); __threadfence(); }
+        if (tid == 0) d_poll(bars, instV, 256);
         __syncthreads();
-        const unsigned short* hq = hreg + p*16384 + db*H2_ + l*16;
+        const unsigned short* hq = hreg + p*16384 + (size_t)b_dec*H2_ + l*16;
         u16x8 h0v = *(const u16x8*)hq;
         u16x8 h1v = *(const u16x8*)(hq + 8);
         float qf[16];
         #pragma unroll
-        for (int c = 0; c < 8; ++c){ qf[c] = bf2f(h0v[c]); qf[8+c] = bf2f(h1v[c]); }
+        for (int e = 0; e < 8; ++e){ qf[e] = bf2f(h0v[e]); qf[8+e] = bf2f(h1v[e]); }
         for (int tp = wv; tp < i; tp += 4){
-          const unsigned short* vr = vbuf + ((size_t)tp*16 + db)*H2_ + l*16;
+          const unsigned short* vr = vbuf + ((size_t)tp*16 + b_dec)*H2_ + l*16;
           u16x8 e0 = *(const u16x8*)vr;
           u16x8 e1 = *(const u16x8*)(vr + 8);
           float sc = 0.f;
           #pragma unroll
-          for (int c = 0; c < 8; ++c) sc += qf[c]*bf2f(e0[c]);
+          for (int e = 0; e < 8; ++e) sc += qf[e]*bf2f(e0[e]);
           #pragma unroll
-          for (int c = 0; c < 8; ++c) sc += qf[8+c]*bf2f(e1[c]);
+          for (int e = 0; e < 8; ++e) sc += qf[8+e]*bf2f(e1[e]);
           #pragma unroll
           for (int o = 1; o < 64; o <<= 1) sc += __shfl_xor(sc, o);
           if (l == 0) dscL[tp] = sc;
         }
         __syncthreads();
-        float scv = (l < i) ? dscL[l] : -1e30f;
-        float m = scv;
-        #pragma unroll
-        for (int o = 1; o < 64; o <<= 1) m = fmaxf(m, __shfl_xor(m, o));
-        float e = (l < i) ? expf(scv - m) : 0.f;
-        float ssum = e;
-        #pragma unroll
-        for (int o = 1; o < 64; o <<= 1) ssum += __shfl_xor(ssum, o);
-        float wgt = e / ssum;
-        float c0_=0.f,c1_=0.f,c2_=0.f,c3_=0.f;
+        float m = -1e30f;
+        for (int tp = 0; tp < i; ++tp) m = fmaxf(m, dscL[tp]);
+        float ssum = 0.f;
+        for (int tp = 0; tp < i; ++tp) ssum += expf(dscL[tp]-m);
+        float inv = 1.f/ssum;
+        float c_ = 0.f;
         for (int tp = 0; tp < i; ++tp){
-          float wt = __shfl(wgt, tp);
-          u16x4 hv = *(const u16x4*)(bufh + ((size_t)tp*16 + db)*H2_ + col);
-          c0_ += wt*bf2f(hv[0]); c1_ += wt*bf2f(hv[1]); c2_ += wt*bf2f(hv[2]); c3_ += wt*bf2f(hv[3]);
+          float wt = expf(dscL[tp]-m)*inv;
+          c_ += wt*bf2f(bufh[((size_t)tp*16 + b_dec)*H2_ + col]);
         }
-        u16x4 o4; o4[0]=f2bf(c0_); o4[1]=f2bf(c1_); o4[2]=f2bf(c2_); o4[3]=f2bf(c3_);
-        *(u16x4*)(xbuf + (size_t)db*1024 + col) = o4;
-        *(u16x4*)(Av + ((size_t)db*TD_ + i)*3072 + 2048 + col) = o4;
-      }
-      __syncthreads();
-      if (tid == 0){ arrive8(barA); poll8(barB, 64); __threadfence(); }
-      __syncthreads();
-    }
+        unsigned short cb = f2bf(c_);
+        xbuf[(size_t)b_dec*H2_ + col] = cb;
+        Av[((size_t)b_dec*TD_ + i)*3072 + 2048 + col] = cb;
+      }
+    }
+    if (tid == 0){ d_arrive(bars, instX); d_poll(bars, instX, 256); }
+    __syncthreads();
+    asm volatile("s_waitcnt vmcnt(0)" ::: "memory");
+    if (w < 64){
+      int b2 = tid >> 4, cs = tid & 15;
+      float val = ctxn[p*16384 + (size_t)b2*H2_ + w*16 + cs] / psumT[p*16 + b2];
+      Av[((size_t)b2*TD_ + i)*3072 + 1024 + w*16 + cs] = f2bf(val);
+    }
+    {
+      float invb = 1.f / psumT[p*16 + (l&15)];
+      int kbase = wv*256;
+      const float* cbase = ctxn + p*16384 + (size_t)(l&15)*H2_ + kbase + (l>>4)*8;
+      #pragma unroll
+      for (int ks = 0; ks < 8; ++ks){
+        float4 v0 = *(const float4*)(cbase + ks*32);
+        float4 v1 = *(const float4*)(cbase + ks*32 + 4);
+        u16x8 afv;
+        afv[0]=f2bf(v0.x*invb); afv[1]=f2bf(v0.y*invb); afv[2]=f2bf(v0.z*invb); afv[3]=f2bf(v0.w*invb);
+        afv[4]=f2bf(v1.x*invb); afv[5]=f2bf(v1.y*invb); afv[6]=f2bf(v1.z*invb); afv[7]=f2bf(v1.w*invb);
+        const char* sbL = myWB + (size_t)(ks>>2)*4096;
+        int k8 = (ks&3)*4 + (l>>4);
+        s16x8 bfr = *(const s16x8*)(sbL + (l&15)*256 + ((k8*16) ^ swz));
+        if (ks & 1) accz1 = __builtin_amdgcn_mfma_f32_16x16x32_bf16((s16x8)afv, bfr, accz1, 0,0,0);
+        else        accz0 = __builtin_amdgcn_mfma_f32_16x16x32_bf16((s16x8)afv, bfr, accz0, 0,0,0);
+      }
+    }
+    {
+      int kbase = wv*256;
+      #pragma unroll
+      for (int ks = 0; ks < 8; ++ks){
+        s16x8 afr = *(const s16x8*)(xbuf + (size_t)(l&15)*H2_ + kbase + ks*32 + (l>>4)*8);
+        const char* sbL = myWB + (size_t)(2 + (ks>>2))*4096;
+        int k8 = (ks&3)*4 + (l>>4);
+        s16x8 bfr = *(const s16x8*)(sbL + (l&15)*256 + ((k8*16) ^ swz));
+        if (ks & 1) accz1 = __builtin_amdgcn_mfma_f32_16x16x32_bf16(afr, bfr, accz1, 0,0,0);
+        else        accz0 = __builtin_amdgcn_mfma_f32_16x16x32_bf16(afr, bfr, accz0, 0,0,0);
+      }
+    }
+    f32x4 accs = accz0 + accz1;
+    if (wv < 2){
+      #pragma unroll
+      for (int j = 0; j < 4; ++j)
+        zl[wv*1024 + ((l>>4)*4+j)*16 + (l&15)] = accs[j];
+    }
+    __syncthreads();
+    if (wv >= 2){
+      #pragma unroll
+      for (int j = 0; j < 4; ++j)
+        zl[(wv-2)*1024 + ((l>>4)*4+j)*16 + (l&15)] += accs[j];
+    }
+    __syncthreads();
+    if (tid < 64){
+      int b2 = tid >> 2, uloc = tid & 3;
+      float zi = zl[b2*16 + 0*4 + uloc] + zl[1024 + b2*16 + 0*4 + uloc];
+      float zf = zl[b2*16 + 1*4 + uloc] + zl[1024 + b2*16 + 1*4 + uloc];
+      float zg = zl[b2*16 + 2*4 + uloc] + zl[1024 + b2*16 + 2*4 + uloc];
+      float zo = zl[b2*16 + 3*4 + uloc] + zl[1024 + b2*16 + 3*4 + uloc];
+      float iv = sigmoidf_(zi), fv = sigmoidf_(zf), gv = tanhf(zg), ov = sigmoidf_(zo);
+      float cc = fv*creg + iv*gv;
+      float hh = ov*tanhf(cc);
+      creg = cc;
+      int u = w*4 + uloc;
+      unsigned short hb2 = f2bf(hh);
+      hreg[((i+1)&1)*16384 + (size_t)b2*H2_ + u] = hb2;
+      Av[((size_t)b2*TD_ + i)*3072 + u] = hb2;
+      bufh[((size_t)i*16 + b2)*H2_ + u] = hb2;
+      if (i == TD_-1){
+        outHC[(size_t)b2*H2_ + u] = hh;
+        outHC[16384 + (size_t)b2*H2_ + u] = cc;
+      }
+    }
+    __syncthreads();
+    if (tid == 0){ d_arrive(bars, instY); d_poll(bars, instY, 256); }
+    __syncthreads();
   }
 }
 
@@ -875,14 +858,14 @@
   char* ws = (char*)d_ws;
 
   size_t o_bars   = 0;
-  size_t o_ctxn   = 327680;
+  size_t o_ctxn   = 397312;
   size_t o_psumT  = o_ctxn + 131072;
   size_t o_xs     = o_psumT + 256;
   size_t o_decemb = o_xs + (size_t)6400*256*2;
   size_t o_Wenc   = o_decemb + (size_t)1024*256*2;
-  size_t o_WhExt  = o_Wenc + (size_t)2*2048*768*2;
-  size_t o_CtxW   = o_WhExt + (size_t)64*163840;
-  size_t o_Wemb   = o_CtxW + (size_t)64*262144;
+  size_t o_RWhh   = o_Wenc + (size_t)2*2048*768*2;
+  size_t o_RWctx  = o_RWhh + (size_t)256*32768;
+  size_t o_Wemb   = o_RWctx + (size_t)256*65536;
   size_t o_zinit  = o_Wemb + (size_t)4096*256*2;
   size_t o_zx     = o_zinit + (size_t)1024*4096*4;
   size_t o_enc    = o_zx + (size_t)2*6400*2048*2;
@@ -902,8 +885,8 @@
   unsigned short* xs    = (unsigned short*)(ws + o_xs);
   unsigned short* decemb= (unsigned short*)(ws + o_decemb);
   unsigned short* Wenc  = (unsigned short*)(ws + o_Wenc);
-  char* WhExt           = ws + o_WhExt;
-  char* CtxW            = ws + o_CtxW;
+  char* RWhh            = ws + o_RWhh;
+  char* RWctx           = ws + o_RWctx;
   unsigned short* Wemb  = (unsigned short*)(ws + o_Wemb);
   float* zinit          = (float*)(ws + o_zinit);
   unsigned short* zx    = (unsigned short*)(ws + o_zx);
@@ -919,9 +902,9 @@
   unsigned short* Av    = (unsigned short*)(ws + o_Av);
 
   hipFuncSetAttribute((const void*)k_encoder, hipFuncAttributeMaxDynamicSharedMemorySize, 90000);
-  hipFuncSetAttribute((const void*)k_decoder, hipFuncAttributeMaxDynamicSharedMemorySize, 160768);
-
-  k_init<<<320, 256, 0, stream>>>(bars, ctxn, psumT);
+  hipFuncSetAttribute((const void*)k_decoder, hipFuncAttributeMaxDynamicSharedMemorySize, DEC_SMEM);
+
+  k_init<<<392, 256, 0, stream>>>(bars, ctxn, psumT);
   k_gather<<<1600, 256, 0, stream>>>(emb, enc_in, xs, TE_);
   k_gather<<<256, 256, 0, stream>>>(emb, dec_in, decemb, TD_);
   k_prep_enc<<<1536, 256, 0, stream>>>(Wih_f, Whh_f, Wih_b, Whh_b, Wenc);
@@ -929,12 +912,12 @@
   k_zinit<<<256, 256, 0, stream>>>(decemb, Wemb, b_d, zinit);
   k_zx<<<1600, 256, 0, stream>>>(xs, Wenc, b_f, b_b, zx);
   k_encoder<<<208, 256, 87296, stream>>>(zx, Wenc, h0, c0, encO, hbuf, h0dec, c0dec, bars,
-                                         Whh_d, W_da, Wih_d, WhExt, CtxW);
+                                         Whh_d, Wih_d, RWhh, RWctx);
   k_penc<<<400, 256, 0, stream>>>(encO, W_ea, Penc);
   k_dec_init<<<64, 256, 0, stream>>>(h0dec, hreg);
-  k_decoder<<<208, 256, 160768, stream>>>(WhExt, CtxW, zinit, Penc, encO, c0dec,
-                                          hreg, xbuf, ctxn, psumT, vbuf, bufh, Av,
-                                          out + (size_t)32768000, bars);
+  k_decoder<<<256, 256, DEC_SMEM, stream>>>(RWhh, RWctx, zinit, Penc, encO, W_da, c0dec,
+                                            hreg, xbuf, ctxn, psumT, vbuf, bufh, Av,
+                                            out + (size_t)32768000, bars);
   k_vocab_gemm<<<2048, 256, 0, stream>>>(Av, W_v, b_v, out);
   k_logsoftmax<<<1024, 256, 0, stream>>>(out);
 }
```

New measurement: 7.228 ms. 1.31x slower.
